# Optimization experiments

Hardware: AMD Instinct MI355X
Metric: run time of the kernel (lower is better)

The kernel has to match this reference:

```python
import jax, jax.numpy as jnp
import numpy as np

B, S, H = 2, 1024, 2048
D = 256          # index_dimension = min(index.embedding_dimension, hidden_size)
R = 32           # LoRA rank
K = 4            # index_k neighbors per query token
N_DB = 100000    # rows in the external index


def setup_inputs() -> dict:
    key = jax.random.key(0)
    ks = jax.random.split(key, 7)
    return {
        "hidden_states": jax.random.normal(ks[0], (B, S, H), jnp.float32),
        "db_keys": jax.random.normal(ks[1], (N_DB, D), jnp.float32),
        "db_values": jax.random.normal(ks[2], (N_DB, D), jnp.float32),
        "wq_in": jax.random.normal(ks[3], (H, R), jnp.float32) * 0.02,
        "wq_out": jax.random.normal(ks[4], (R, D), jnp.float32) * 0.02,
        "wv_in": jax.random.normal(ks[5], (D, R), jnp.float32) * 0.02,
        "wv_out": jax.random.normal(ks[6], (R, H), jnp.float32) * 0.02,
    }


def reference(hidden_states, db_keys, db_values, wq_in, wq_out, wv_in, wv_out):
    b, s, h = hidden_states.shape
    d = wq_out.shape[1]
    # query LoRA projection: hidden -> r -> index_dim
    q = (hidden_states @ wq_in) @ wq_out            # [B, S, D]

    # external k-NN lookup (exact L2 top-k over index table), no_grad in torch
    qf = q.reshape(b * s, d)                        # [B*S, D]
    qn = jnp.sum(qf * qf, axis=-1, keepdims=True)   # [B*S, 1]
    kn = jnp.sum(db_keys * db_keys, axis=-1)        # [N_DB]
    dist = qn - 2.0 * (qf @ db_keys.T) + kn[None, :]  # [B*S, N_DB]
    _, idx = jax.lax.top_k(-dist, K)                # [B*S, K] nearest neighbors

    # gather KV and reshape to [B, S*K, D] (matches torch view calls)
    kv_key = jax.lax.stop_gradient(db_keys[idx]).reshape(b, s * K, d)
    kv_val = jax.lax.stop_gradient(db_values[idx]).reshape(b, s * K, d)

    # SDPA, is_causal=True with Lq != Lk: top-left aligned tril mask (j <= i)
    scale = 1.0 / np.sqrt(d).astype(np.float32)
    scores = jnp.einsum('bqd,bkd->bqk', q, kv_key) * scale  # [B, S, S*K]
    mask = jnp.arange(s * K)[None, :] <= jnp.arange(s)[:, None]
    scores = jnp.where(mask[None, :, :], scores, jnp.finfo(scores.dtype).min)
    attn = jax.nn.softmax(scores, axis=-1)
    out = jnp.einsum('bqk,bkd->bqd', attn, kv_val)  # [B, S, D]

    # value LoRA projection: index_dim -> r -> hidden
    return (out @ wv_in) @ wv_out                   # [B, S, H]
```

## Files before the change

### kernel.cpp

```cpp
#include <hip/hip_runtime.h>
#include <cfloat>

#define B_   2
#define S_   1024
#define H_   2048
#define D_   256
#define R_   32
#define K_   4
#define NDB_ 100000

#define TSEL 256
#define NSEL (B_ * TSEL)

#define NCHUNK     61
#define CHUNK_ROWS 1664
#define TILES      13
#define NT         128
#define MT         64
#define KC         64
#define LSTR       68

#define NEG_INF  (-3.0e38f)
#define IDX_MAX  0x7fffffff

#define TQ 4

#define OFF_Q     0
#define OFF_KN    0x200000
#define OFF_PS    0x280000
#define OFF_PI    0x300000
#define OFF_IDX   0x380000
#define OFF_CAND  0x3A0000
#define OFF_KVT   0x400000
#define OFF_AO    0x600000
#define OFF_KVV   0x800000
#define OFF_DBK16 0xA00000

typedef unsigned short ushort_t;
typedef unsigned int   uint_t;
typedef __attribute__((ext_vector_type(8)))  __bf16 bf16x8;
typedef __attribute__((ext_vector_type(16))) float  f32x16;

__device__ __forceinline__ void ins4(float sc, int n, float s[4], int id[4]) {
  if (sc > s[3] || (sc == s[3] && n < id[3])) {
    s[3] = sc; id[3] = n;
#pragma unroll
    for (int k = 3; k > 0; --k) {
      if (s[k] > s[k - 1] || (s[k] == s[k - 1] && id[k] < id[k - 1])) {
        float ts = s[k]; s[k] = s[k - 1]; s[k - 1] = ts;
        int ti = id[k]; id[k] = id[k - 1]; id[k - 1] = ti;
      }
    }
  }
}

__device__ __forceinline__ uint_t bfpack(float a, float b) {
  uint_t ua = __float_as_uint(a), ub = __float_as_uint(b);
  ua = (ua + 0x7fffu + ((ua >> 16) & 1u)) >> 16;
  ub = (ub + 0x7fffu + ((ub >> 16) & 1u)) >> 16;
  return ua | (ub << 16);
}

__global__ __launch_bounds__(256) void k_compute_q(
    const float* __restrict__ hidden, const float* __restrict__ wq_in,
    const float* __restrict__ wq_out, float* __restrict__ q) {
  __shared__ float hrow[H_];
  __shared__ float part[8][R_];
  __shared__ float q1[R_];
  const int m = blockIdx.x;
  const int t = threadIdx.x;
  const float* hp = hidden + (size_t)m * H_;
  ((float4*)hrow)[t]       = ((const float4*)hp)[t];
  ((float4*)hrow)[t + 256] = ((const float4*)hp)[t + 256];
  __syncthreads();
  const int r = t & 31, c = t >> 5;
  float p = 0.f;
#pragma unroll 4
  for (int e = c * 256; e < c * 256 + 256; ++e)
    p = fmaf(hrow[e], wq_in[(size_t)e * R_ + r], p);
  part[c][r] = p;
  __syncthreads();
  if (t < R_) {
    float s = 0.f;
#pragma unroll
    for (int cc = 0; cc < 8; ++cc) s += part[cc][t];
    q1[t] = s;
  }
  __syncthreads();
  float acc = 0.f;
#pragma unroll
  for (int rr = 0; rr < R_; ++rr) acc = fmaf(q1[rr], wq_out[rr * D_ + t], acc);
  q[(size_t)m * D_ + t] = acc;
}

__global__ __launch_bounds__(256) void k_kn_cvtT(const float* __restrict__ dbk,
                                                 float* __restrict__ kn,
                                                 ushort_t* __restrict__ dbk16T) {
  const int n32 = blockIdx.x;
  const int t = threadIdx.x;
  const int r = t >> 3, tc = t & 7;
  const int n = n32 * 32 + r;
  const float* rp = dbk + (size_t)n * D_ + tc * 32;
  uint4* dst = (uint4*)dbk16T;
  float s = 0.f;
#pragma unroll
  for (int cc = 0; cc < 4; ++cc) {
    const int c = tc * 4 + cc;
    const float4 a = ((const float4*)rp)[cc * 2];
    const float4 b = ((const float4*)rp)[cc * 2 + 1];
    uint4 pk;
    pk.x = bfpack(a.x, a.y); pk.y = bfpack(a.z, a.w);
    pk.z = bfpack(b.x, b.y); pk.w = bfpack(b.z, b.w);
    dst[(size_t)(n32 * 16 + (c >> 1)) * 64 + (c & 1) * 32 + r] = pk;
    s += a.x*a.x + a.y*a.y + a.z*a.z + a.w*a.w;
    s += b.x*b.x + b.y*b.y + b.z*b.z + b.w*b.w;
  }
  s += __shfl_down(s, 4, 8);
  s += __shfl_down(s, 2, 8);
  s += __shfl_down(s, 1, 8);
  if (tc == 0) kn[n] = s;
}

__global__ __launch_bounds__(256) void k_kn(const float* __restrict__ dbk,
                                            float* __restrict__ kn) {
  const int w = threadIdx.x >> 6, l = threadIdx.x & 63;
  const int n = blockIdx.x * 4 + w;
  if (n >= NDB_) return;
  const float4 v = ((const float4*)(dbk + (size_t)n * D_))[l];
  float s = v.x * v.x + v.y * v.y + v.z * v.z + v.w * v.w;
#pragma unroll
  for (int off = 32; off; off >>= 1) s += __shfl_down(s, off);
  if (l == 0) kn[n] = s;
}

__global__ __launch_bounds__(256, 2) void k_knn_mfma(
    const float* __restrict__ q, const ushort_t* __restrict__ dbk16T,
    const float* __restrict__ kn, float* __restrict__ pscore,
    int* __restrict__ pidx) {
  __shared__ __align__(16) char smem[32768 + CHUNK_ROWS * 4];
  ushort_t* sA  = (ushort_t*)smem;
  float*    knL = (float*)(smem + 32768);

  const int fid = blockIdx.x;
  const int chunk = (fid & 7) + 8 * ((fid >> 3) & 7);
  const int qb = fid >> 6;
  if (chunk >= NCHUNK) return;

  const int tid = threadIdx.x;
  const int wv = tid >> 6, ln = tid & 63;
  const int lm = ln & 31, lh = ln >> 5;
  const int row_base = chunk * CHUNK_ROWS;

  {
    const int m = tid & 63, cg = tid >> 6;
    const int sq = qb * MT + m;
    const float* qp = q + ((size_t)((sq >> 8) * S_ + (sq & 255))) * D_;
#pragma unroll
    for (int cc = 0; cc < 8; ++cc) {
      const int c = cg * 8 + cc;
      const float4 v0 = *(const float4*)(qp + c * 8);
      const float4 v1 = *(const float4*)(qp + c * 8 + 4);
      uint4 pk;
      pk.x = bfpack(v0.x, v0.y); pk.y = bfpack(v0.z, v0.w);
      pk.z = bfpack(v1.x, v1.y); pk.w = bfpack(v1.z, v1.w);
      *(uint4*)&sA[(m * 32 + (c ^ (m & 7))) * 8] = pk;
    }
  }
  for (int j = tid; j < CHUNK_ROWS; j += 256) {
    int rr = row_base + j; if (rr >= NDB_) rr = NDB_ - 1;
    knL[j] = kn[rr];
  }
  __syncthreads();

  float s40[4], s41[4]; int i40[4], i41[4];
#pragma unroll
  for (int k = 0; k < 4; ++k) {
    s40[k] = NEG_INF; i40[k] = IDX_MAX;
    s41[k] = NEG_INF; i41[k] = IDX_MAX;
  }

  const int sw = lm & 7;
  const int abase0 = lm * 32;
  const int abase1 = (32 + lm) * 32;
  const int nbase = wv * 32 + 4 * lh;

  for (int tile = 0; tile < TILES; ++tile) {
    const int row0 = row_base + tile * NT;
    if (row0 >= NDB_) break;
    const int nw = row0 + wv * 32;
    if (nw >= NDB_) continue;

    f32x16 acc0, acc1;
#pragma unroll
    for (int r = 0; r < 16; ++r) { acc0[r] = 0.f; acc1[r] = 0.f; }

    const ushort_t* gw = dbk16T + (size_t)(nw >> 5) * 8192 + (size_t)ln * 8;
#pragma unroll
    for (int ks = 0; ks < 16; ++ks) {
      const bf16x8 bb = *(const bf16x8*)(gw + ks * 512);
      const int cs = (2 * ks + lh) ^ sw;
      const bf16x8 a0 = *(const bf16x8*)&sA[(abase0 + cs) * 8];
      const bf16x8 a1 = *(const bf16x8*)&sA[(abase1 + cs) * 8];
      acc0 = __builtin_amdgcn_mfma_f32_32x32x16_bf16(bb, a0, acc0, 0, 0, 0);
      acc1 = __builtin_amdgcn_mfma_f32_32x32x16_bf16(bb, a1, acc1, 0, 0, 0);
    }

#pragma unroll
    for (int g = 0; g < 4; ++g) {
      float v0[4], v1[4]; int nn[4];
#pragma unroll
      for (int j = 0; j < 4; ++j) {
        const int r = g * 4 + j;
        const int off = (r & 3) + 8 * (r >> 2);
        const int nloc = nbase + off;
        const float knv = knL[tile * 128 + nloc];
        const int n = row0 + nloc;
        nn[j] = n;
        const float x0 = fmaf(2.f, acc0[r], -knv);
        const float x1 = fmaf(2.f, acc1[r], -knv);
        const bool ok = n < NDB_;
        v0[j] = ok ? x0 : NEG_INF;
        v1[j] = ok ? x1 : NEG_INF;
      }
      const float m0 = fmaxf(fmaxf(v0[0], v0[1]), fmaxf(v0[2], v0[3]));
      if (m0 >= s40[3]) {
#pragma unroll
        for (int j = 0; j < 4; ++j) ins4(v0[j], nn[j], s40, i40);
      }
      const float m1 = fmaxf(fmaxf(v1[0], v1[1]), fmaxf(v1[2], v1[3]));
      if (m1 >= s41[3]) {
#pragma unroll
        for (int j = 0; j < 4; ++j) ins4(v1[j], nn[j], s41, i41);
      }
    }
  }

  __syncthreads();
  float* cs = (float*)smem;
  int*   ci = (int*)(smem + 8192);
  {
    const int st = wv * 2 + lh;
#pragma unroll
    for (int k = 0; k < 4; ++k) {
      cs[(lm * 8 + st) * 4 + k]        = s40[k];
      ci[(lm * 8 + st) * 4 + k]        = i40[k];
      cs[((32 + lm) * 8 + st) * 4 + k] = s41[k];
      ci[((32 + lm) * 8 + st) * 4 + k] = i41[k];
    }
  }
  __syncthreads();
  if (tid < 64) {
    float fs[4]; int fi[4];
#pragma unroll
    for (int k = 0; k < 4; ++k) { fs[k] = NEG_INF; fi[k] = IDX_MAX; }
    for (int c = 0; c < 32; ++c)
      ins4(cs[tid * 32 + c], ci[tid * 32 + c], fs, fi);
    const int sq = qb * MT + tid;
    float* po = pscore + ((size_t)sq * NCHUNK + chunk) * 4;
    int*   io = pidx   + ((size_t)sq * NCHUNK + chunk) * 4;
#pragma unroll
    for (int k = 0; k < 4; ++k) { po[k] = fs[k]; io[k] = fi[k]; }
  }
}

__global__ __launch_bounds__(256) void k_knn_partial(
    const float* __restrict__ q, const float* __restrict__ dbk,
    const float* __restrict__ kn, float* __restrict__ pscore,
    int* __restrict__ pidx) {
  __shared__ float smem[3 * KC * LSTR];
  float* sA  = smem;
  float* sB0 = smem + KC * LSTR;
  float* sB1 = smem + 2 * KC * LSTR;
  const int tid = threadIdx.x;
  const int tx = tid & 15, ty = tid >> 4;
  const int chunk = blockIdx.x, qb = blockIdx.y;
  const int arq = tid >> 2;
  const int aqd = (tid & 3) * 4;
  const int brk = tid >> 1;
  const int bh  = tid & 1;
  const int bcol = ((brk >> 3) << 2) | (brk & 3);
  float* sBw = (brk & 4) ? sB1 : sB0;
  const int sq_a = qb * MT + arq;
  const float* qsrc = q + ((size_t)((sq_a >> 8) * S_ + (sq_a & 255))) * D_;
  float s4[4][4]; int i4[4][4];
#pragma unroll
  for (int a = 0; a < 4; ++a)
#pragma unroll
    for (int b = 0; b < 4; ++b) { s4[a][b] = NEG_INF; i4[a][b] = IDX_MAX; }
  const int row_base = chunk * CHUNK_ROWS;
  for (int tile = 0; tile < TILES; ++tile) {
    const int row0 = row_base + tile * NT;
    if (row0 >= NDB_) break;
    int krow = row0 + brk; if (krow >= NDB_) krow = NDB_ - 1;
    const float* ksrc = dbk + (size_t)krow * D_;
    float acc[4][8];
#pragma unroll
    for (int a = 0; a < 4; ++a)
#pragma unroll
      for (int b = 0; b < 8; ++b) acc[a][b] = 0.f;
    for (int kc = 0; kc < 4; ++kc) {
      __syncthreads();
#pragma unroll
      for (int p = 0; p < 4; ++p) {
        const int kkl = p * 16 + aqd;
        const float4 v = *(const float4*)(qsrc + kc * KC + kkl);
        sA[(kkl + 0) * LSTR + arq] = v.x;
        sA[(kkl + 1) * LSTR + arq] = v.y;
        sA[(kkl + 2) * LSTR + arq] = v.z;
        sA[(kkl + 3) * LSTR + arq] = v.w;
      }
#pragma unroll
      for (int p = 0; p < 8; ++p) {
        const int kkl = bh * 32 + p * 4;
        const float4 v = *(const float4*)(ksrc + kc * KC + kkl);
        sBw[(kkl + 0) * LSTR + bcol] = v.x;
        sBw[(kkl + 1) * LSTR + bcol] = v.y;
        sBw[(kkl + 2) * LSTR + bcol] = v.z;
        sBw[(kkl + 3) * LSTR + bcol] = v.w;
      }
      __syncthreads();
#pragma unroll 4
      for (int kk = 0; kk < KC; ++kk) {
        const float4 a  = *(const float4*)&sA [kk * LSTR + ty * 4];
        const float4 b0 = *(const float4*)&sB0[kk * LSTR + tx * 4];
        const float4 b1 = *(const float4*)&sB1[kk * LSTR + tx * 4];
        const float av[4] = {a.x, a.y, a.z, a.w};
        const float bv[8] = {b0.x, b0.y, b0.z, b0.w, b1.x, b1.y, b1.z, b1.w};
#pragma unroll
        for (int qi = 0; qi < 4; ++qi)
#pragma unroll
          for (int nj = 0; nj < 8; ++nj)
            acc[qi][nj] = fmaf(av[qi], bv[nj], acc[qi][nj]);
      }
    }
#pragma unroll
    for (int nj = 0; nj < 8; ++nj) {
      const int n = row0 + tx * 8 + nj;
      if (n < NDB_) {
        const float knj = kn[n];
        ins4(2.f * acc[0][nj] - knj, n, s4[0], i4[0]);
        ins4(2.f * acc[1][nj] - knj, n, s4[1], i4[1]);
        ins4(2.f * acc[2][nj] - knj, n, s4[2], i4[2]);
        ins4(2.f * acc[3][nj] - knj, n, s4[3], i4[3]);
      }
    }
  }
  __syncthreads();
  float* cs = smem;
  int*   ci = (int*)(smem + 64 * 65);
#pragma unroll
  for (int qi = 0; qi < 4; ++qi)
#pragma unroll
    for (int k = 0; k < 4; ++k) {
      cs[(ty * 4 + qi) * 65 + tx * 4 + k] = s4[qi][k];
      ci[(ty * 4 + qi) * 65 + tx * 4 + k] = i4[qi][k];
    }
  __syncthreads();
  if (tid < 64) {
    float fs[4]; int fi[4];
#pragma unroll
    for (int k = 0; k < 4; ++k) { fs[k] = NEG_INF; fi[k] = IDX_MAX; }
    for (int c = 0; c < 64; ++c)
      ins4(cs[tid * 65 + c], ci[tid * 65 + c], fs, fi);
    const int sq = qb * MT + tid;
    float* po = pscore + ((size_t)sq * NCHUNK + chunk) * 4;
    int*   io = pidx   + ((size_t)sq * NCHUNK + chunk) * 4;
#pragma unroll
    for (int k = 0; k < 4; ++k) { po[k] = fs[k]; io[k] = fi[k]; }
  }
}

template <int RANKS>
__device__ __forceinline__ void merge_top(const float* __restrict__ pscore,
                                          const int* __restrict__ pidx,
                                          int* __restrict__ outp) {
  const int sq = blockIdx.x, l = threadIdx.x;
  float s4[4]; int i4[4];
#pragma unroll
  for (int k = 0; k < 4; ++k) { s4[k] = NEG_INF; i4[k] = IDX_MAX; }
  for (int c = l; c < NCHUNK * 4; c += 64)
    ins4(pscore[(size_t)sq * NCHUNK * 4 + c], pidx[(size_t)sq * NCHUNK * 4 + c], s4, i4);
#pragma unroll
  for (int r = 0; r < RANKS; ++r) {
    float s = s4[0]; int i = i4[0];
#pragma unroll
    for (int off = 32; off; off >>= 1) {
      float so = __shfl_down(s, off); int io = __shfl_down(i, off);
      if (so > s || (so == s && io < i)) { s = so; i = io; }
    }
    const float sw = __shfl(s, 0); const int iw = __shfl(i, 0);
    if (l == 0) outp[sq * RANKS + r] = iw;
    if (s4[0] == sw && i4[0] == iw) {
      s4[0] = s4[1]; i4[0] = i4[1];
      s4[1] = s4[2]; i4[1] = i4[2];
      s4[2] = s4[3]; i4[2] = i4[3];
      s4[3] = NEG_INF; i4[3] = IDX_MAX;
    }
  }
}

__global__ __launch_bounds__(64) void k_knn_merge4(const float* __restrict__ ps,
                                                   const int* __restrict__ pi,
                                                   int* __restrict__ knn_idx) {
  merge_top<4>(ps, pi, knn_idx);
}
__global__ __launch_bounds__(64) void k_knn_merge16(const float* __restrict__ ps,
                                                    const int* __restrict__ pi,
                                                    int* __restrict__ cand) {
  merge_top<16>(ps, pi, cand);
}

__global__ __launch_bounds__(256) void k_rescore(const float* __restrict__ q,
                                                 const float* __restrict__ dbk,
                                                 const float* __restrict__ kn,
                                                 const int* __restrict__ cand,
                                                 int* __restrict__ knn_idx) {
  __shared__ float scs[16];
  __shared__ int   sci[16];
  const int sq = blockIdx.x, wv = threadIdx.x >> 6, l = threadIdx.x & 63;
  const float* qp = q + ((size_t)((sq >> 8) * S_ + (sq & 255))) * D_;
  const float4 qv = ((const float4*)qp)[l];
  for (int cc = wv; cc < 16; cc += 4) {
    const int n = cand[sq * 16 + cc];
    const float4 kv = ((const float4*)(dbk + (size_t)n * D_))[l];
    float s = qv.x * kv.x + qv.y * kv.y + qv.z * kv.z + qv.w * kv.w;
#pragma unroll
    for (int off = 32; off; off >>= 1) s += __shfl_down(s, off);
    if (l == 0) { scs[cc] = 2.f * s - kn[n]; sci[cc] = n; }
  }
  __syncthreads();
  if (threadIdx.x == 0) {
    float s4[4]; int i4[4];
#pragma unroll
    for (int k = 0; k < 4; ++k) { s4[k] = NEG_INF; i4[k] = IDX_MAX; }
#pragma unroll
    for (int c = 0; c < 16; ++c) ins4(scs[c], sci[c], s4, i4);
#pragma unroll
    for (int k = 0; k < 4; ++k) knn_idx[sq * 4 + k] = i4[k];
  }
}

__global__ __launch_bounds__(256) void k_gather(const float* __restrict__ dbk,
                                                const float* __restrict__ dbv,
                                                const int* __restrict__ knn_idx,
                                                float* __restrict__ kvT,
                                                float* __restrict__ kvV) {
  const int b = blockIdx.x >> 6, j0 = (blockIdx.x & 63) * 16;
  const int w = threadIdx.x >> 6, l = threadIdx.x & 63;
  float* dstT = kvT + (size_t)b * D_ * 1024;
  float* dstV = kvV + (size_t)b * 1024 * D_;
  for (int jj = w; jj < 16; jj += 4) {
    const int j = j0 + jj;
    const int row = knn_idx[b * 1024 + j];
    const float4 kv = ((const float4*)(dbk + (size_t)row * D_))[l];
    dstT[(4 * l + 0) * 1024 + j] = kv.x;
    dstT[(4 * l + 1) * 1024 + j] = kv.y;
    dstT[(4 * l + 2) * 1024 + j] = kv.z;
    dstT[(4 * l + 3) * 1024 + j] = kv.w;
    const float4 vv = ((const float4*)(dbv + (size_t)row * D_))[l];
    ((float4*)(dstV + (size_t)j * D_))[l] = vv;
  }
}

template <int CMAX>
__device__ __forceinline__ void qk_dots(const float* __restrict__ kb, int t,
                                        const float (*qrow)[D_], float a[4][TQ]) {
#pragma unroll 2
  for (int d = 0; d < D_; d += 4) {
    float qv[TQ][4];
#pragma unroll
    for (int q = 0; q < TQ; ++q) {
      const float4 v = *(const float4*)&qrow[q][d];
      qv[q][0] = v.x; qv[q][1] = v.y; qv[q][2] = v.z; qv[q][3] = v.w;
    }
#pragma unroll
    for (int dd = 0; dd < 4; ++dd) {
      float kv[CMAX];
#pragma unroll
      for (int c = 0; c < CMAX; ++c)
        kv[c] = kb[(size_t)(d + dd) * 1024 + c * 256 + t];
#pragma unroll
      for (int c = 0; c < CMAX; ++c)
#pragma unroll
        for (int q = 0; q < TQ; ++q)
          a[c][q] = fmaf(qv[q][dd], kv[c], a[c][q]);
    }
  }
}

__global__ __launch_bounds__(256) void k_attn(const float* __restrict__ qarr,
                                              const float* __restrict__ kvT,
                                              const float* __restrict__ kvV,
                                              float* __restrict__ attout) {
  __shared__ float qrow[TQ][D_];
  __shared__ float attw[TQ][1024];
  __shared__ float pvred[4][TQ][D_];
  __shared__ float redm[4][TQ], reds[4][TQ];

  const int fid = blockIdx.x;
  const int b = fid & 1;
  const int g = fid >> 1;
  const int h = g >> 1;
  const int grp = (g & 1) ? (255 - h) : h;
  const int i0 = grp * TQ;
  const int t = threadIdx.x;
  const int w = t >> 6, l = t & 63;
  const int nkmax = i0 + TQ;
  const int cmax = (nkmax + 255) >> 8;

  {
    const float4 v = ((const float4*)(qarr + ((size_t)b * S_ + i0 + w) * D_))[l];
    float4 sv;
    sv.x = v.x * 0.0625f; sv.y = v.y * 0.0625f;
    sv.z = v.z * 0.0625f; sv.w = v.w * 0.0625f;
    ((float4*)&qrow[w][0])[l] = sv;
  }
  __syncthreads();

  const float* kb = kvT + (size_t)b * D_ * 1024;
  float a[4][TQ];
#pragma unroll
  for (int c = 0; c < 4; ++c)
#pragma unroll
    for (int q = 0; q < TQ; ++q) a[c][q] = 0.f;
  switch (cmax) {
    case 1: qk_dots<1>(kb, t, qrow, a); break;
    case 2: qk_dots<2>(kb, t, qrow, a); break;
    case 3: qk_dots<3>(kb, t, qrow, a); break;
    default: qk_dots<4>(kb, t, qrow, a); break;
  }
#pragma unroll
  for (int c = 0; c < 4; ++c)
    if (c < cmax)
#pragma unroll
      for (int q = 0; q < TQ; ++q)
        if (c * 256 + t > i0 + q) a[c][q] = NEG_INF;

  float M[TQ];
#pragma unroll
  for (int q = 0; q < TQ; ++q) {
    float m = NEG_INF;
    for (int c = 0; c < cmax; ++c) m = fmaxf(m, a[c][q]);
#pragma unroll
    for (int off = 32; off; off >>= 1) m = fmaxf(m, __shfl_down(m, off));
    if (l == 0) redm[w][q] = m;
  }
  __syncthreads();
#pragma unroll
  for (int q = 0; q < TQ; ++q)
    M[q] = fmaxf(fmaxf(redm[0][q], redm[1][q]), fmaxf(redm[2][q], redm[3][q]));
  float inv[TQ];
#pragma unroll
  for (int q = 0; q < TQ; ++q) {
    float s = 0.f;
    for (int c = 0; c < cmax; ++c) {
      const float p = (a[c][q] > 0.5f * NEG_INF) ? __expf(a[c][q] - M[q]) : 0.f;
      a[c][q] = p; s += p;
    }
#pragma unroll
    for (int off = 32; off; off >>= 1) s += __shfl_down(s, off);
    if (l == 0) reds[w][q] = s;
  }
  __syncthreads();
#pragma unroll
  for (int q = 0; q < TQ; ++q)
    inv[q] = 1.f / (reds[0][q] + reds[1][q] + reds[2][q] + reds[3][q]);
  for (int c = 0; c < cmax; ++c)
#pragma unroll
    for (int q = 0; q < TQ; ++q)
      attw[q][c * 256 + t] = a[c][q] * inv[q];
  __syncthreads();

  const float* vb = kvV + (size_t)b * 1024 * D_;
  float4 acc[TQ];
#pragma unroll
  for (int q = 0; q < TQ; ++q) acc[q] = make_float4(0.f, 0.f, 0.f, 0.f);
#pragma unroll 2
  for (int j = w; j < nkmax; j += 4) {
    const float4 v = ((const float4*)(vb + (size_t)j * D_))[l];
#pragma unroll
    for (int q = 0; q < TQ; ++q) {
      const float p = attw[q][j];
      acc[q].x = fmaf(p, v.x, acc[q].x);
      acc[q].y = fmaf(p, v.y, acc[q].y);
      acc[q].z = fmaf(p, v.z, acc[q].z);
      acc[q].w = fmaf(p, v.w, acc[q].w);
    }
  }
#pragma unroll
  for (int q = 0; q < TQ; ++q) ((float4*)&pvred[w][q][0])[l] = acc[q];
  __syncthreads();
  {
    const int q = t >> 6;
    float4 s = make_float4(0.f, 0.f, 0.f, 0.f);
#pragma unroll
    for (int ww = 0; ww < 4; ++ww) {
      const float4 p = ((const float4*)&pvred[ww][q][0])[l];
      s.x += p.x; s.y += p.y; s.z += p.z; s.w += p.w;
    }
    ((float4*)(attout + ((size_t)b * S_ + i0 + q) * D_))[l] = s;
  }
}

__global__ __launch_bounds__(256) void k_out(const float* __restrict__ attout,
                                             const float* __restrict__ wv_in,
                                             const float* __restrict__ wv_out,
                                             float* __restrict__ y) {
  __shared__ float row[D_];
  __shared__ float part[8][R_];
  __shared__ float t32[R_];
  const int m = blockIdx.x, t = threadIdx.x;
  row[t] = attout[(size_t)m * D_ + t];
  __syncthreads();
  const int r = t & 31, c = t >> 5;
  float p = 0.f;
#pragma unroll
  for (int d = c * 32; d < c * 32 + 32; ++d)
    p = fmaf(row[d], wv_in[d * R_ + r], p);
  part[c][r] = p;
  __syncthreads();
  if (t < R_) {
    float s = 0.f;
#pragma unroll
    for (int cc = 0; cc < 8; ++cc) s += part[cc][t];
    t32[t] = s;
  }
  __syncthreads();
  for (int hh = t; hh < H_; hh += 256) {
    float a = 0.f;
#pragma unroll
    for (int rr = 0; rr < R_; ++rr) a = fmaf(t32[rr], wv_out[rr * H_ + hh], a);
    y[(size_t)m * H_ + hh] = a;
  }
}

extern "C" void kernel_launch(void* const* d_in, const int* in_sizes, int n_in,
                              void* d_out, int out_size, void* d_ws, size_t ws_size,
                              hipStream_t stream) {
  const float* hidden  = (const float*)d_in[0];
  const float* db_keys = (const float*)d_in[1];
  const float* db_vals = (const float*)d_in[2];
  const float* wq_in   = (const float*)d_in[3];
  const float* wq_out  = (const float*)d_in[4];
  const float* wv_in   = (const float*)d_in[5];
  const float* wv_out  = (const float*)d_in[6];
  float* out = (float*)d_out;

  char* ws = (char*)d_ws;
  float*    q      = (float*)(ws + OFF_Q);
  float*    kn     = (float*)(ws + OFF_KN);
  float*    ps     = (float*)(ws + OFF_PS);
  int*      pi     = (int*)  (ws + OFF_PI);
  int*      idx    = (int*)  (ws + OFF_IDX);
  int*      cand   = (int*)  (ws + OFF_CAND);
  float*    kvT    = (float*)(ws + OFF_KVT);
  float*    attout = (float*)(ws + OFF_AO);
  float*    kvV    = (float*)(ws + OFF_KVV);
  ushort_t* dbk16  = (ushort_t*)(ws + OFF_DBK16);

  const size_t need = (size_t)OFF_DBK16 + (size_t)NDB_ * D_ * 2;

  k_compute_q<<<B_ * S_, 256, 0, stream>>>(hidden, wq_in, wq_out, q);
  if (ws_size >= need) {
    k_kn_cvtT<<<NDB_ / 32, 256, 0, stream>>>(db_keys, kn, dbk16);
    k_knn_mfma<<<512, 256, 0, stream>>>(q, dbk16, kn, ps, pi);
    k_knn_merge16<<<NSEL, 64, 0, stream>>>(ps, pi, cand);
    k_rescore<<<NSEL, 256, 0, stream>>>(q, db_keys, kn, cand, idx);
  } else {
    k_kn<<<(NDB_ + 3) / 4, 256, 0, stream>>>(db_keys, kn);
    k_knn_partial<<<dim3(NCHUNK, 8), 256, 0, stream>>>(q, db_keys, kn, ps, pi);
    k_knn_merge4<<<NSEL, 64, 0, stream>>>(ps, pi, idx);
  }
  k_gather<<<2 * 64, 256, 0, stream>>>(db_keys, db_vals, idx, kvT, kvV);
  k_attn<<<512, 256, 0, stream>>>(q, kvT, kvV, attout);
  k_out<<<B_ * S_, 256, 0, stream>>>(attout, wv_in, wv_out, out);
}
```

Measured before the change: 451.6 us.

## Split kNN into smaller chunks, raise occupancy, and stage bf16 key transpose through LDS

The kNN scoring kernel now uses 112 chunks of 896 rows instead of 61 chunks of 1664 rows, launched as 896 blocks with an XCD-aware block mapping and a minimum of 4 blocks per CU instead of 2. This is meant to fill the GPU better and remove idle padding blocks. The db_keys bf16 conversion/transpose kernel now stages rows through XOR-swizzled shared memory so that both the global reads and the transposed global writes are coalesced. Workspace offsets are rearranged to fit the larger partial-score buffers. The trade-offs are more partial candidates for the merge kernel to process and tighter register limits in the MFMA kernel.

```diff
diff --git a/kernel.cpp b/kernel.cpp
--- a/kernel.cpp
+++ b/kernel.cpp
@@ -12,9 +12,9 @@
 #define TSEL 256
 #define NSEL (B_ * TSEL)
 
-#define NCHUNK     61
-#define CHUNK_ROWS 1664
-#define TILES      13
+#define NCHUNK     112
+#define CHUNK_ROWS 896
+#define TILES      7
 #define NT         128
 #define MT         64
 #define KC         64
@@ -28,12 +28,12 @@
 #define OFF_Q     0
 #define OFF_KN    0x200000
 #define OFF_PS    0x280000
-#define OFF_PI    0x300000
-#define OFF_IDX   0x380000
-#define OFF_CAND  0x3A0000
-#define OFF_KVT   0x400000
-#define OFF_AO    0x600000
-#define OFF_KVV   0x800000
+#define OFF_PI    0x360000
+#define OFF_KVV   0x280000
+#define OFF_KVT   0x480000
+#define OFF_AO    0x680000
+#define OFF_IDX   0x880000
+#define OFF_CAND  0x890000
 #define OFF_DBK16 0xA00000
 
 typedef unsigned short ushort_t;
@@ -96,29 +96,43 @@
 __global__ __launch_bounds__(256) void k_kn_cvtT(const float* __restrict__ dbk,
                                                  float* __restrict__ kn,
                                                  ushort_t* __restrict__ dbk16T) {
+  __shared__ float sT[32 * 256];
   const int n32 = blockIdx.x;
   const int t = threadIdx.x;
-  const int r = t >> 3, tc = t & 7;
-  const int n = n32 * 32 + r;
-  const float* rp = dbk + (size_t)n * D_ + tc * 32;
-  uint4* dst = (uint4*)dbk16T;
-  float s = 0.f;
-#pragma unroll
-  for (int cc = 0; cc < 4; ++cc) {
-    const int c = tc * 4 + cc;
-    const float4 a = ((const float4*)rp)[cc * 2];
-    const float4 b = ((const float4*)rp)[cc * 2 + 1];
-    uint4 pk;
-    pk.x = bfpack(a.x, a.y); pk.y = bfpack(a.z, a.w);
-    pk.z = bfpack(b.x, b.y); pk.w = bfpack(b.z, b.w);
-    dst[(size_t)(n32 * 16 + (c >> 1)) * 64 + (c & 1) * 32 + r] = pk;
-    s += a.x*a.x + a.y*a.y + a.z*a.z + a.w*a.w;
-    s += b.x*b.x + b.y*b.y + b.z*b.z + b.w*b.w;
-  }
-  s += __shfl_down(s, 4, 8);
-  s += __shfl_down(s, 2, 8);
-  s += __shfl_down(s, 1, 8);
-  if (tc == 0) kn[n] = s;
+  {
+    const int r = t >> 3, tc = t & 7;
+    const float* rp = dbk + (size_t)(n32 * 32 + r) * D_;
+    float s = 0.f;
+#pragma unroll
+    for (int k = 0; k < 8; ++k) {
+      const int sl = tc + 8 * k;
+      const float4 v = ((const float4*)rp)[sl];
+      *(float4*)&sT[(r * 64 + (sl ^ (r & 7))) * 4] = v;
+      s += v.x * v.x + v.y * v.y + v.z * v.z + v.w * v.w;
+    }
+    s += __shfl_down(s, 4, 8);
+    s += __shfl_down(s, 2, 8);
+    s += __shfl_down(s, 1, 8);
+    if (tc == 0) kn[n32 * 32 + r] = s;
+  }
+  __syncthreads();
+  {
+    const int l = t & 63, w = t >> 6;
+    const int row = l & 31, hc = l >> 5;
+    uint4* dst = (uint4*)dbk16T + (size_t)n32 * 1024;
+#pragma unroll
+    for (int kk = 0; kk < 4; ++kk) {
+      const int ks = kk * 4 + w;
+      const int c = 2 * ks + hc;
+      const int s0 = (2 * c) ^ (row & 7), s1 = (2 * c + 1) ^ (row & 7);
+      const float4 a = *(const float4*)&sT[(row * 64 + s0) * 4];
+      const float4 b = *(const float4*)&sT[(row * 64 + s1) * 4];
+      uint4 pk;
+      pk.x = bfpack(a.x, a.y); pk.y = bfpack(a.z, a.w);
+      pk.z = bfpack(b.x, b.y); pk.w = bfpack(b.z, b.w);
+      dst[(size_t)ks * 64 + l] = pk;
+    }
+  }
 }
 
 __global__ __launch_bounds__(256) void k_kn(const float* __restrict__ dbk,
@@ -133,7 +147,7 @@
   if (l == 0) kn[n] = s;
 }
 
-__global__ __launch_bounds__(256, 2) void k_knn_mfma(
+__global__ __launch_bounds__(256, 4) void k_knn_mfma(
     const float* __restrict__ q, const ushort_t* __restrict__ dbk16T,
     const float* __restrict__ kn, float* __restrict__ pscore,
     int* __restrict__ pidx) {
@@ -142,9 +156,9 @@
   float*    knL = (float*)(smem + 32768);
 
   const int fid = blockIdx.x;
-  const int chunk = (fid & 7) + 8 * ((fid >> 3) & 7);
-  const int qb = fid >> 6;
-  if (chunk >= NCHUNK) return;
+  const int xcd = fid & 7, idx8 = fid >> 3;
+  const int chunk = xcd + 8 * (idx8 % 14);
+  const int qb = idx8 / 14;
 
   const int tid = threadIdx.x;
   const int wv = tid >> 6, ln = tid & 63;
@@ -663,7 +677,7 @@
   k_compute_q<<<B_ * S_, 256, 0, stream>>>(hidden, wq_in, wq_out, q);
   if (ws_size >= need) {
     k_kn_cvtT<<<NDB_ / 32, 256, 0, stream>>>(db_keys, kn, dbk16);
-    k_knn_mfma<<<512, 256, 0, stream>>>(q, dbk16, kn, ps, pi);
+    k_knn_mfma<<<NCHUNK * 8, 256, 0, stream>>>(q, dbk16, kn, ps, pi);
     k_knn_merge16<<<NSEL, 64, 0, stream>>>(ps, pi, cand);
     k_rescore<<<NSEL, 256, 0, stream>>>(q, db_keys, kn, cand, idx);
   } else {
```

After: 441.4 us. 1.02x faster.
